# Performance work log

Measured on AMD Instinct MI355X. Metric: run time of the kernel, lower is better.

The kernel has to match this reference:

```python
import jax, jax.numpy as jnp
import numpy as np
from jax import lax

B, C, OUT, H, W = 4, 64, 64, 128, 128
BN_EPS = 1e-5
DN = ('NCHW', 'OIHW', 'NCHW')


def conv3x3(x, w, pad=1, dil=1, groups=1):
    return lax.conv_general_dilated(
        x, w, window_strides=(1, 1), padding=[(pad, pad), (pad, pad)],
        rhs_dilation=(dil, dil), dimension_numbers=DN,
        feature_group_count=groups)


def setup_inputs() -> dict:
    key = jax.random.key(0)
    ks = jax.random.split(key, 10)
    return {
        'x': jax.random.normal(ks[0], (B, C, H, W), jnp.float32),
        'kernel': jax.random.normal(ks[1], (B, 3, OUT, C, 3, 3), jnp.float32) * 0.05,
        'conv_mask_w': jax.random.normal(ks[2], (3, C, 3, 3), jnp.float32) * 0.05,
        'conv_mask_b': jnp.zeros((3,), jnp.float32),
        'conv_out_w': jax.random.normal(ks[3], (OUT, OUT * 4, 3, 3), jnp.float32) * 0.05,
        'conv_out_b': jnp.zeros((OUT,), jnp.float32),
        'bn_gamma': jnp.ones((OUT,), jnp.float32),
        'bn_beta': jnp.zeros((OUT,), jnp.float32),
        'bn_mean': jax.random.normal(ks[4], (OUT,), jnp.float32) * 0.1,
        'bn_var': jax.random.uniform(ks[5], (OUT,), jnp.float32, 0.5, 1.5),
    }


def reference(x, kernel, conv_mask_w, conv_mask_b, conv_out_w, conv_out_b,
              bn_gamma, bn_beta, bn_mean, bn_var):
    b, c, h, w = x.shape
    out_ch = conv_out_w.shape[0]

    # mask branch: conv -> Softmax2d (softmax over channel dim)
    masks = conv3x3(x, conv_mask_w) + conv_mask_b[None, :, None, None]
    masks = jax.nn.softmax(masks, axis=1)  # [b, 3, h, w]

    # per-sample mask-weighted copies: [b, 3, c, h, w] -> grouped-conv layout
    xm = (x[:, None, :, :, :] * masks[:, :, None, :, :]).reshape(1, b * 3 * c, h, w)

    # all four branches use the SAME kernel slice kernel[:, 0:3] (as in the source)
    kw = kernel[:, 0:3].reshape(-1, c, 3, 3)  # [b*3*out, c, 3, 3]

    def branch(dil):
        y = conv3x3(xm, kw, pad=dil, dil=dil, groups=b * 3)
        return y.reshape(b, 3, out_ch, h, w).sum(axis=1)  # sum over the 3 masks

    cat = jnp.concatenate([branch(1), branch(3), branch(5), branch(7)], axis=1)

    out = conv3x3(cat, conv_out_w) + conv_out_b[None, :, None, None]
    # BatchNorm2d in eval mode (running stats)
    inv = bn_gamma / jnp.sqrt(bn_var + BN_EPS)
    out = out * inv[None, :, None, None] + (bn_beta - bn_mean * inv)[None, :, None, None]
    out = jax.nn.relu(out)
    return (out, masks)
```

## Files before the change

### kernel.cpp

```cpp
#include <hip/hip_runtime.h>
#include <math.h>

typedef __bf16 bf16;
typedef __bf16 bf16x8 __attribute__((ext_vector_type(8)));
typedef __bf16 bf16x4 __attribute__((ext_vector_type(4)));
typedef float  f32x4  __attribute__((ext_vector_type(4)));

#define HW        16384
#define OUT_ELEMS 4194304

#define XM_ROW    (142 * 64)
#define XM_PLANE  (142 * XM_ROW)
#define CAT_ROW   (130 * 256)
#define CAT_PLANE (130 * CAT_ROW)

#define LPX 72

__global__ void k_mask1(const float* __restrict__ x, const float* __restrict__ mw,
                        float* __restrict__ part) {
  int y = blockIdx.x, b = blockIdx.y, cg = blockIdx.z;
  int tx = threadIdx.x;
  float a0 = 0.f, a1 = 0.f, a2 = 0.f;
#pragma unroll
  for (int ci = 0; ci < 8; ++ci) {
    int c = cg * 8 + ci;
    const float* xp = x + ((size_t)(b * 64 + c)) * HW;
    const float* w0 = mw + (0 * 64 + c) * 9;
    const float* w1 = mw + (1 * 64 + c) * 9;
    const float* w2 = mw + (2 * 64 + c) * 9;
#pragma unroll
    for (int ky = 0; ky < 3; ++ky) {
      int yy = y + ky - 1;
      if ((unsigned)yy >= 128u) continue;
#pragma unroll
      for (int kx = 0; kx < 3; ++kx) {
        int xx = tx + kx - 1;
        if ((unsigned)xx >= 128u) continue;
        float xv = xp[yy * 128 + xx];
        a0 += xv * w0[ky * 3 + kx];
        a1 += xv * w1[ky * 3 + kx];
        a2 += xv * w2[ky * 3 + kx];
      }
    }
  }
  size_t base = (size_t)((b * 8 + cg) * 3) * HW + y * 128 + tx;
  part[base]          = a0;
  part[base + HW]     = a1;
  part[base + 2 * HW] = a2;
}

__global__ void k_xmt(const float* __restrict__ x, const float* __restrict__ part,
                      const float* __restrict__ mb, float* __restrict__ masks,
                      bf16* __restrict__ xm_p,
                      const float* __restrict__ kern, const float* __restrict__ w2,
                      bf16* __restrict__ kern_t, bf16* __restrict__ w2_t) {
  int yp = blockIdx.x;
  int m = blockIdx.y, b = blockIdx.z;
  int t = threadIdx.x;

  {
    const int NK  = 442368;
    const int NW2 = 147456;
    int bid2 = yp + 142 * (m + 3 * b);
#pragma unroll
    for (int it = 0; it < 2; ++it) {
      int idx = (bid2 + it * 1704) * 256 + t;
      if (idx < NK) {
        int j    = idx & 7;
        int lane = (idx >> 3) & 63;
        int km   = (idx >> 9) & 7;
        int tap  = (idx >> 12) % 9;
        int bm   = idx / 36864;
        int o = (km >> 1) * 16 + (lane & 15);
        int c = (km & 1) * 32 + (lane >> 4) * 8 + j;
        kern_t[idx] = (bf16)kern[(((bm * 64 + o) * 64 + c) * 9) + tap];
      } else if (idx < NK + NW2) {
        int j = idx - NK;
        int j8   = j & 7;
        int lane = (j >> 3) & 63;
        int km   = (j >> 9) & 7;
        int cq   = (j >> 12) & 3;
        int tap  = j >> 14;
        int oc = (km >> 1) * 16 + (lane & 15);
        int ch = cq * 64 + (km & 1) * 32 + (lane >> 4) * 8 + j8;
        w2_t[j] = (bf16)w2[(oc * 256 + ch) * 9 + tap];
      }
    }
  }

  bf16* prow = xm_p + (size_t)(b * 3 + m) * XM_PLANE + (size_t)yp * XM_ROW;
  bf16x8 z = {};
  if (yp < 7 || yp >= 135) {
#pragma unroll
    for (int i = 0; i < 5; ++i) {
      int u = i * 256 + t;
      if (u < 1136) ((bf16x8*)prow)[u] = z;
    }
    return;
  }
  if (t < 56) ((bf16x8*)prow)[t] = z;
  else if (t < 112) ((bf16x8*)(prow + 135 * 64))[t - 56] = z;

  int y = yp - 7;
  __shared__ float tile[64 * 130];
  __shared__ float mrow_s[128];
#pragma unroll
  for (int i = 0; i < 32; ++i) {
    int u = i * 256 + t;
    int c = u >> 7, xx = u & 127;
    tile[c * 130 + xx] = x[((size_t)(b * 64 + c)) * HW + y * 128 + xx];
  }
  if (t < 128) {
    float a0 = mb[0], a1 = mb[1], a2 = mb[2];
    int off = y * 128 + t;
#pragma unroll
    for (int cg = 0; cg < 8; ++cg) {
      size_t base = (size_t)((b * 8 + cg) * 3) * HW + off;
      a0 += part[base];
      a1 += part[base + HW];
      a2 += part[base + 2 * HW];
    }
    float mx = fmaxf(a0, fmaxf(a1, a2));
    float e0 = __expf(a0 - mx), e1 = __expf(a1 - mx), e2 = __expf(a2 - mx);
    float inv = 1.0f / (e0 + e1 + e2);
    float v0 = e0 * inv, v1 = e1 * inv, v2 = e2 * inv;
    mrow_s[t] = (m == 0) ? v0 : (m == 1) ? v1 : v2;
    if (m == 0) {
      size_t mbase = ((size_t)b * 3) * HW + off;
      masks[mbase]          = v0;
      masks[mbase + HW]     = v1;
      masks[mbase + 2 * HW] = v2;
    }
  }
  __syncthreads();
  bf16* orow = prow + 7 * 64;
#pragma unroll
  for (int i = 0; i < 4; ++i) {
    int u = i * 256 + t;
    int cg = u & 7, xx = u >> 3;
    float mv = mrow_s[xx];
    bf16x8 v;
#pragma unroll
    for (int j = 0; j < 8; ++j)
      v[j] = (bf16)(tile[(cg * 8 + j) * 130 + xx] * mv);
    *(bf16x8*)(orow + xx * 64 + cg * 8) = v;
  }
}

__global__ __launch_bounds__(256, 2) void k_branch(const bf16* __restrict__ xm_p,
                                                   const bf16* __restrict__ kern_t,
                                                   bf16* __restrict__ cat_p) {
  __shared__ bf16 sb[4][2][78 * 64];
  int bid = blockIdx.x;
  {
    int id = bid * 256 + threadIdx.x;
    if (id < 4 * 16512) {
      int plane = id / 16512, j = id % 16512;
      bf16* base = cat_p + (size_t)plane * CAT_PLANE;
      bf16x8 zv = {};
      if (j < 8320) {
        int row = (j / 4160) * 129;
        int off = (j % 4160) * 8;
        *(bf16x8*)(base + (size_t)row * CAT_ROW + off) = zv;
      } else {
        int k = j - 8320;
        int row = 1 + (k >> 6);
        int idx2 = k & 63;
        int col = (idx2 >> 5) * 129;
        int ch8 = (idx2 & 31) * 8;
        *(bf16x8*)(base + (size_t)row * CAT_ROW + col * 256 + ch8) = zv;
      }
    }
  }
  int xcd = bid & 7;
  int i   = bid >> 3;
  int b   = xcd >> 1;
  int di  = ((xcd & 1) << 1) | (i & 1);
  int ypr = i >> 1;
  int d   = 1 + 2 * di;
  int t    = threadIdx.x;
  int lane = t & 63;
  int wave = t >> 6;
  int yr   = wave >> 1;
  int wh   = wave & 1;
  int y    = ypr * 2 + yr;
  int lanelo = lane & 15;
  int quad = lane >> 4;

  const bf16* plane0 = xm_p + (size_t)(b * 3) * XM_PLANE;
  const bf16* wb0    = kern_t + (size_t)(b * 27) * 4096 + lane * 8;
  const int gp0 = wh * 64 + 7 - d;

  bf16* mysb0 = &sb[wave][0][0];
  bf16* mysb1 = &sb[wave][1][0];

  bf16x8 sreg[10];
  {
    const bf16* s0 = plane0 + (size_t)(y + 7 - d) * XM_ROW + gp0 * 64;
#pragma unroll
    for (int r = 0; r < 10; ++r) {
      int u = r * 64 + lane;
      if (u < 624) sreg[r] = *(const bf16x8*)(s0 + u * 8);
    }
#pragma unroll
    for (int r = 0; r < 10; ++r) {
      int u = r * 64 + lane;
      if (u < 624) {
        int px = u >> 3, sl = u & 7;
        *(bf16x8*)(mysb0 + px * 64 + ((sl ^ (px & 7)) << 3)) = sreg[r];
      }
    }
    const bf16* s1 = plane0 + (size_t)(y + 7) * XM_ROW + gp0 * 64;
#pragma unroll
    for (int r = 0; r < 10; ++r) {
      int u = r * 64 + lane;
      if (u < 624) sreg[r] = *(const bf16x8*)(s1 + u * 8);
    }
  }

  f32x4 acc[4][4] = {};

#pragma unroll
  for (int p = 0; p < 9; ++p) {
    int m = p / 3, ky = p % 3;
    bf16x8 areg[3][2][4];
    const bf16* wtap = wb0 + (size_t)(m * 9 + ky * 3) * 4096;
#pragma unroll
    for (int kx = 0; kx < 3; ++kx)
#pragma unroll
      for (int kci = 0; kci < 2; ++kci)
#pragma unroll
        for (int mt = 0; mt < 4; ++mt)
          areg[kx][kci][mt] = *(const bf16x8*)(wtap + kx * 4096 + (mt * 2 + kci) * 512);

    if (p < 8) {
      bf16* wbuf = ((p + 1) & 1) ? mysb1 : mysb0;
#pragma unroll
      for (int r = 0; r < 10; ++r) {
        int u = r * 64 + lane;
        if (u < 624) {
          int px = u >> 3, sl = u & 7;
          *(bf16x8*)(wbuf + px * 64 + ((sl ^ (px & 7)) << 3)) = sreg[r];
        }
      }
    }
    if (p < 7) {
      int pn = p + 2;
      int mn = pn / 3, kyn = pn % 3;
      const bf16* sn = plane0 + (size_t)mn * XM_PLANE
                     + (size_t)(y + 7 + d * (kyn - 1)) * XM_ROW + gp0 * 64;
#pragma unroll
      for (int r = 0; r < 10; ++r) {
        int u = r * 64 + lane;
        if (u < 624) sreg[r] = *(const bf16x8*)(sn + u * 8);
      }
    }
    const bf16* rbuf = (p & 1) ? mysb1 : mysb0;
#pragma unroll
    for (int kx = 0; kx < 3; ++kx) {
      int lpx0 = lanelo + d * kx;
      int p7   = lpx0 & 7;
#pragma unroll
      for (int kci = 0; kci < 2; ++kci) {
        int swsl = ((quad + 4 * kci) ^ p7) << 3;
        bf16x8 bv[4];
#pragma unroll
        for (int nt = 0; nt < 4; ++nt)
          bv[nt] = *(const bf16x8*)(rbuf + (lpx0 + nt * 16) * 64 + swsl);
        __builtin_amdgcn_s_setprio(1);
#pragma unroll
        for (int mt = 0; mt < 4; ++mt)
#pragma unroll
          for (int nt = 0; nt < 4; ++nt)
            acc[mt][nt] = __builtin_amdgcn_mfma_f32_16x16x32_bf16(areg[kx][kci][mt], bv[nt], acc[mt][nt], 0, 0, 0);
        __builtin_amdgcn_s_setprio(0);
      }
    }
  }

  bf16* cp = cat_p + (size_t)b * CAT_PLANE + (size_t)(y + 1) * CAT_ROW + di * 64;
#pragma unroll
  for (int mt = 0; mt < 4; ++mt) {
#pragma unroll
    for (int nt = 0; nt < 4; ++nt) {
      int px = wh * 64 + nt * 16 + lanelo;
      bf16x4 v;
#pragma unroll
      for (int r = 0; r < 4; ++r) v[r] = (bf16)acc[mt][nt][r];
      *(bf16x4*)(cp + (size_t)(px + 1) * 256 + (mt * 16 + quad * 4)) = v;
    }
  }
}

__global__ __launch_bounds__(256, 2) void k_final(const bf16* __restrict__ cat_p,
                                                  const bf16* __restrict__ w2_t,
                                                  const float* __restrict__ cb,
                                                  const float* __restrict__ gamma,
                                                  const float* __restrict__ beta,
                                                  const float* __restrict__ mean,
                                                  const float* __restrict__ var,
                                                  float* __restrict__ out) {
  __shared__ bf16 sb[4][2][40 * LPX];
  int bid = blockIdx.x;
  int xcd = bid & 7;
  int b   = xcd >> 1;
  int y   = ((bid >> 3) << 1) | (xcd & 1);
  int t    = threadIdx.x;
  int lane = t & 63;
  int wq   = t >> 6;
  int lanelo = lane & 15;
  int quad = lane >> 4;

  const bf16* cb2 = cat_p + (size_t)b * CAT_PLANE + (size_t)(wq * 32) * 256;
  const bf16* wb0 = w2_t + lane * 8;

  bf16* mysb0 = &sb[wq][0][0];
  bf16* mysb1 = &sb[wq][1][0];

  bf16x8 sreg[5];
  {
    const bf16* s0 = cb2 + (size_t)y * CAT_ROW;
#pragma unroll
    for (int r = 0; r < 5; ++r) {
      int u = r * 64 + lane;
      sreg[r] = *(const bf16x8*)(s0 + (u >> 3) * 256 + (u & 7) * 8);
    }
#pragma unroll
    for (int r = 0; r < 5; ++r) {
      int u = r * 64 + lane;
      *(bf16x8*)(mysb0 + (u >> 3) * LPX + (u & 7) * 8) = sreg[r];
    }
    const bf16* s1 = cb2 + (size_t)(y + 1) * CAT_ROW;
#pragma unroll
    for (int r = 0; r < 5; ++r) {
      int u = r * 64 + lane;
      sreg[r] = *(const bf16x8*)(s1 + (u >> 3) * 256 + (u & 7) * 8);
    }
  }

  f32x4 acc[4][2] = {};

#pragma unroll
  for (int p = 0; p < 12; ++p) {
    int cq = p / 3, ky = p % 3;
    bf16x8 areg[3][2][4];
#pragma unroll
    for (int kx = 0; kx < 3; ++kx) {
      const bf16* wt = wb0 + (size_t)(((ky * 3 + kx) * 4 + cq) * 8) * 512;
#pragma unroll
      for (int kci = 0; kci < 2; ++kci)
#pragma unroll
        for (int mt = 0; mt < 4; ++mt)
          areg[kx][kci][mt] = *(const bf16x8*)(wt + (mt * 2 + kci) * 512);
    }

    if (p < 11) {
      bf16* wbuf = ((p + 1) & 1) ? mysb1 : mysb0;
#pragma unroll
      for (int r = 0; r < 5; ++r) {
        int u = r * 64 + lane;
        *(bf16x8*)(wbuf + (u >> 3) * LPX + (u & 7) * 8) = sreg[r];
      }
    }
    if (p < 10) {
      int pn = p + 2;
      int cqn = pn / 3, kyn = pn % 3;
      const bf16* sn = cb2 + (size_t)(y + kyn) * CAT_ROW + cqn * 64;
#pragma unroll
      for (int r = 0; r < 5; ++r) {
        int u = r * 64 + lane;
        sreg[r] = *(const bf16x8*)(sn + (u >> 3) * 256 + (u & 7) * 8);
      }
    }
    const bf16* rbuf = (p & 1) ? mysb1 : mysb0;
#pragma unroll
    for (int kx = 0; kx < 3; ++kx) {
      int lpx0 = lanelo + kx;
#pragma unroll
      for (int kci = 0; kci < 2; ++kci) {
        bf16x8 bv[2];
#pragma unroll
        for (int nt = 0; nt < 2; ++nt)
          bv[nt] = *(const bf16x8*)(rbuf + (lpx0 + nt * 16) * LPX + quad * 8 + kci * 32);
        __builtin_amdgcn_s_setprio(1);
#pragma unroll
        for (int mt = 0; mt < 4; ++mt)
#pragma unroll
          for (int nt = 0; nt < 2; ++nt)
            acc[mt][nt] = __builtin_amdgcn_mfma_f32_16x16x32_bf16(areg[kx][kci][mt], bv[nt], acc[mt][nt], 0, 0, 0);
        __builtin_amdgcn_s_setprio(0);
      }
    }
  }

#pragma unroll
  for (int mt = 0; mt < 4; ++mt) {
#pragma unroll
    for (int nt = 0; nt < 2; ++nt) {
      int px = wq * 32 + nt * 16 + lanelo;
#pragma unroll
      for (int r = 0; r < 4; ++r) {
        int oc = mt * 16 + quad * 4 + r;
        float inv = gamma[oc] * rsqrtf(var[oc] + 1e-5f);
        float v = (acc[mt][nt][r] + cb[oc]) * inv + beta[oc] - mean[oc] * inv;
        out[((size_t)(b * 64 + oc)) * HW + y * 128 + px] = fmaxf(v, 0.0f);
      }
    }
  }
}

extern "C" void kernel_launch(void* const* d_in, const int* in_sizes, int n_in,
                              void* d_out, int out_size, void* d_ws, size_t ws_size,
                              hipStream_t stream) {
  const float* x     = (const float*)d_in[0];
  const float* kern  = (const float*)d_in[1];
  const float* mw    = (const float*)d_in[2];
  const float* mb    = (const float*)d_in[3];
  const float* w2    = (const float*)d_in[4];
  const float* cb    = (const float*)d_in[5];
  const float* gamma = (const float*)d_in[6];
  const float* beta  = (const float*)d_in[7];
  const float* mean  = (const float*)d_in[8];
  const float* var   = (const float*)d_in[9];

  float* out   = (float*)d_out;
  float* masks = out + OUT_ELEMS;

  char* ws = (char*)d_ws;
  bf16* xm_p   = (bf16*)(ws);
  bf16* cat_p  = (bf16*)(ws + 30971904);
  bf16* kern_t = (bf16*)(ws + 65583104);
  bf16* w2_t   = (bf16*)(ws + 66467840);
  float* part  = (float*)(ws + 30971904);

  k_mask1<<<dim3(128, 4, 8), 128, 0, stream>>>(x, mw, part);
  k_xmt<<<dim3(142, 3, 4), 256, 0, stream>>>(x, part, mb, masks, xm_p, kern, w2, kern_t, w2_t);
  k_branch<<<1024, 256, 0, stream>>>(xm_p, kern_t, cat_p);
  k_final<<<512, 256, 0, stream>>>(cat_p, w2_t, cb, gamma, beta, mean, var, out);
}
```

Measured before the change: 227.8 us.

## Widen final conv wave tile to 64 pixels and load weights per kx

The final 3x3 conv now gives each wave 64 output pixels instead of 32, with four waves covering two output rows per block. The grid is halved, and each weight register load now feeds twice as many MFMAs. In both conv kernels the per-tap weight fragments are loaded inside the kx loop rather than all at once, which shrinks live registers to fit the larger accumulator. The cost is more LDS per block (66-pixel staging), fewer blocks, and weight loads that are less far ahead of their use.

```diff
diff --git a/kernel.cpp b/kernel.cpp
--- a/kernel.cpp
+++ b/kernel.cpp
@@ -223,15 +223,7 @@
 #pragma unroll
   for (int p = 0; p < 9; ++p) {
     int m = p / 3, ky = p % 3;
-    bf16x8 areg[3][2][4];
     const bf16* wtap = wb0 + (size_t)(m * 9 + ky * 3) * 4096;
-#pragma unroll
-    for (int kx = 0; kx < 3; ++kx)
-#pragma unroll
-      for (int kci = 0; kci < 2; ++kci)
-#pragma unroll
-        for (int mt = 0; mt < 4; ++mt)
-          areg[kx][kci][mt] = *(const bf16x8*)(wtap + kx * 4096 + (mt * 2 + kci) * 512);
 
     if (p < 8) {
       bf16* wbuf = ((p + 1) & 1) ? mysb1 : mysb0;
@@ -258,6 +250,12 @@
     const bf16* rbuf = (p & 1) ? mysb1 : mysb0;
 #pragma unroll
     for (int kx = 0; kx < 3; ++kx) {
+      bf16x8 areg[2][4];
+#pragma unroll
+      for (int kci = 0; kci < 2; ++kci)
+#pragma unroll
+        for (int mt = 0; mt < 4; ++mt)
+          areg[kci][mt] = *(const bf16x8*)(wtap + kx * 4096 + (mt * 2 + kci) * 512);
       int lpx0 = lanelo + d * kx;
       int p7   = lpx0 & 7;
 #pragma unroll
@@ -272,7 +270,7 @@
         for (int mt = 0; mt < 4; ++mt)
 #pragma unroll
           for (int nt = 0; nt < 4; ++nt)
-            acc[mt][nt] = __builtin_amdgcn_mfma_f32_16x16x32_bf16(areg[kx][kci][mt], bv[nt], acc[mt][nt], 0, 0, 0);
+            acc[mt][nt] = __builtin_amdgcn_mfma_f32_16x16x32_bf16(areg[kci][mt], bv[nt], acc[mt][nt], 0, 0, 0);
         __builtin_amdgcn_s_setprio(0);
       }
     }
@@ -300,66 +298,59 @@
                                                   const float* __restrict__ mean,
                                                   const float* __restrict__ var,
                                                   float* __restrict__ out) {
-  __shared__ bf16 sb[4][2][40 * LPX];
+  __shared__ bf16 sb[4][2][66 * LPX];
   int bid = blockIdx.x;
   int xcd = bid & 7;
   int b   = xcd >> 1;
-  int y   = ((bid >> 3) << 1) | (xcd & 1);
+  int ypr = ((bid >> 3) << 1) | (xcd & 1);
   int t    = threadIdx.x;
   int lane = t & 63;
-  int wq   = t >> 6;
+  int wave = t >> 6;
+  int yr   = wave >> 1;
+  int wh   = wave & 1;
+  int y    = ypr * 2 + yr;
   int lanelo = lane & 15;
   int quad = lane >> 4;
 
-  const bf16* cb2 = cat_p + (size_t)b * CAT_PLANE + (size_t)(wq * 32) * 256;
+  const bf16* cb2 = cat_p + (size_t)b * CAT_PLANE + (size_t)(wh * 64) * 256;
   const bf16* wb0 = w2_t + lane * 8;
 
-  bf16* mysb0 = &sb[wq][0][0];
-  bf16* mysb1 = &sb[wq][1][0];
-
-  bf16x8 sreg[5];
+  bf16* mysb0 = &sb[wave][0][0];
+  bf16* mysb1 = &sb[wave][1][0];
+
+  bf16x8 sreg[9];
   {
     const bf16* s0 = cb2 + (size_t)y * CAT_ROW;
 #pragma unroll
-    for (int r = 0; r < 5; ++r) {
-      int u = r * 64 + lane;
-      sreg[r] = *(const bf16x8*)(s0 + (u >> 3) * 256 + (u & 7) * 8);
-    }
-#pragma unroll
-    for (int r = 0; r < 5; ++r) {
-      int u = r * 64 + lane;
-      *(bf16x8*)(mysb0 + (u >> 3) * LPX + (u & 7) * 8) = sreg[r];
+    for (int r = 0; r < 9; ++r) {
+      int u = r * 64 + lane;
+      if (u < 528) sreg[r] = *(const bf16x8*)(s0 + (u >> 3) * 256 + (u & 7) * 8);
+    }
+#pragma unroll
+    for (int r = 0; r < 9; ++r) {
+      int u = r * 64 + lane;
+      if (u < 528) *(bf16x8*)(mysb0 + (u >> 3) * LPX + (u & 7) * 8) = sreg[r];
     }
     const bf16* s1 = cb2 + (size_t)(y + 1) * CAT_ROW;
 #pragma unroll
-    for (int r = 0; r < 5; ++r) {
-      int u = r * 64 + lane;
-      sreg[r] = *(const bf16x8*)(s1 + (u >> 3) * 256 + (u & 7) * 8);
-    }
-  }
-
-  f32x4 acc[4][2] = {};
+    for (int r = 0; r < 9; ++r) {
+      int u = r * 64 + lane;
+      if (u < 528) sreg[r] = *(const bf16x8*)(s1 + (u >> 3) * 256 + (u & 7) * 8);
+    }
+  }
+
+  f32x4 acc[4][4] = {};
 
 #pragma unroll
   for (int p = 0; p < 12; ++p) {
     int cq = p / 3, ky = p % 3;
-    bf16x8 areg[3][2][4];
-#pragma unroll
-    for (int kx = 0; kx < 3; ++kx) {
-      const bf16* wt = wb0 + (size_t)(((ky * 3 + kx) * 4 + cq) * 8) * 512;
-#pragma unroll
-      for (int kci = 0; kci < 2; ++kci)
-#pragma unroll
-        for (int mt = 0; mt < 4; ++mt)
-          areg[kx][kci][mt] = *(const bf16x8*)(wt + (mt * 2 + kci) * 512);
-    }
 
     if (p < 11) {
       bf16* wbuf = ((p + 1) & 1) ? mysb1 : mysb0;
 #pragma unroll
-      for (int r = 0; r < 5; ++r) {
+      for (int r = 0; r < 9; ++r) {
         int u = r * 64 + lane;
-        *(bf16x8*)(wbuf + (u >> 3) * LPX + (u & 7) * 8) = sreg[r];
+        if (u < 528) *(bf16x8*)(wbuf + (u >> 3) * LPX + (u & 7) * 8) = sreg[r];
       }
     }
     if (p < 10) {
@@ -367,27 +358,34 @@
       int cqn = pn / 3, kyn = pn % 3;
       const bf16* sn = cb2 + (size_t)(y + kyn) * CAT_ROW + cqn * 64;
 #pragma unroll
-      for (int r = 0; r < 5; ++r) {
+      for (int r = 0; r < 9; ++r) {
         int u = r * 64 + lane;
-        sreg[r] = *(const bf16x8*)(sn + (u >> 3) * 256 + (u & 7) * 8);
+        if (u < 528) sreg[r] = *(const bf16x8*)(sn + (u >> 3) * 256 + (u & 7) * 8);
       }
     }
     const bf16* rbuf = (p & 1) ? mysb1 : mysb0;
 #pragma unroll
     for (int kx = 0; kx < 3; ++kx) {
+      bf16x8 areg[2][4];
+      const bf16* wt = wb0 + (size_t)(((ky * 3 + kx) * 4 + cq) * 8) * 512;
+#pragma unroll
+      for (int kci = 0; kci < 2; ++kci)
+#pragma unroll
+        for (int mt = 0; mt < 4; ++mt)
+          areg[kci][mt] = *(const bf16x8*)(wt + (mt * 2 + kci) * 512);
       int lpx0 = lanelo + kx;
 #pragma unroll
       for (int kci = 0; kci < 2; ++kci) {
-        bf16x8 bv[2];
-#pragma unroll
-        for (int nt = 0; nt < 2; ++nt)
+        bf16x8 bv[4];
+#pragma unroll
+        for (int nt = 0; nt < 4; ++nt)
           bv[nt] = *(const bf16x8*)(rbuf + (lpx0 + nt * 16) * LPX + quad * 8 + kci * 32);
         __builtin_amdgcn_s_setprio(1);
 #pragma unroll
         for (int mt = 0; mt < 4; ++mt)
 #pragma unroll
-          for (int nt = 0; nt < 2; ++nt)
-            acc[mt][nt] = __builtin_amdgcn_mfma_f32_16x16x32_bf16(areg[kx][kci][mt], bv[nt], acc[mt][nt], 0, 0, 0);
+          for (int nt = 0; nt < 4; ++nt)
+            acc[mt][nt] = __builtin_amdgcn_mfma_f32_16x16x32_bf16(areg[kci][mt], bv[nt], acc[mt][nt], 0, 0, 0);
         __builtin_amdgcn_s_setprio(0);
       }
     }
@@ -396,8 +394,8 @@
 #pragma unroll
   for (int mt = 0; mt < 4; ++mt) {
 #pragma unroll
-    for (int nt = 0; nt < 2; ++nt) {
-      int px = wq * 32 + nt * 16 + lanelo;
+    for (int nt = 0; nt < 4; ++nt) {
+      int px = wh * 64 + nt * 16 + lanelo;
 #pragma unroll
       for (int r = 0; r < 4; ++r) {
         int oc = mt * 16 + quad * 4 + r;
@@ -436,5 +434,5 @@
   k_mask1<<<dim3(128, 4, 8), 128, 0, stream>>>(x, mw, part);
   k_xmt<<<dim3(142, 3, 4), 256, 0, stream>>>(x, part, mb, masks, xm_p, kern, w2, kern_t, w2_t);
   k_branch<<<1024, 256, 0, stream>>>(xm_p, kern_t, cat_p);
-  k_final<<<512, 256, 0, stream>>>(cat_p, w2_t, cb, gamma, beta, mean, var, out);
+  k_final<<<256, 256, 0, stream>>>(cat_p, w2_t, cb, gamma, beta, mean, var, out);
 }
```

Measured after the change: 210.3 us. 7.7% less time.
